# Kernel tuning notes

Hardware: AMD Instinct MI355X
Metric: run time of the kernel (lower is better)

The kernel has to match this reference:

```python
import jax, jax.numpy as jnp
import numpy as np

D_MODEL = 1024
H = 16
D_HEAD = D_MODEL // H  # 64
RANK = 32
ALPHA = 1.0


def _lora_linear(x, W, b, dW, dB):
    # merged weight: W + alpha * (dB @ dW), then x @ W_merged.T + b
    Wm = W + ALPHA * (dB @ dW)
    return x @ Wm.T + b


def setup_inputs() -> dict:
    key = jax.random.key(0)
    ks = jax.random.split(key, 20)
    inp = {"x": jax.random.normal(ks[0], (2, 2048, D_MODEL), dtype=jnp.float32)}
    i = 1
    for name in ("q", "k", "v", "o"):
        inp[f"{name}_W"] = jax.random.normal(ks[i], (D_MODEL, D_MODEL), dtype=jnp.float32) * 0.02; i += 1
        inp[f"{name}_b"] = jnp.zeros((D_MODEL,), dtype=jnp.float32)
        inp[f"{name}_dW"] = jax.random.normal(ks[i], (RANK, D_MODEL), dtype=jnp.float32) * 0.01; i += 1
        inp[f"{name}_dB"] = jax.random.normal(ks[i], (D_MODEL, RANK), dtype=jnp.float32) * 0.01; i += 1
    return inp


def reference(x, q_W, q_b, q_dW, q_dB, k_W, k_b, k_dW, k_dB,
              v_W, v_b, v_dW, v_dB, o_W, o_b, o_dW, o_dB):
    b_s, n, _ = x.shape
    # LoRA-merged QKV projections
    q = _lora_linear(x, q_W, q_b, q_dW, q_dB).reshape(b_s, n, H, D_HEAD)
    k = _lora_linear(x, k_W, k_b, k_dW, k_dB).reshape(b_s, n, H, D_HEAD)
    v = _lora_linear(x, v_W, v_b, v_dW, v_dB).reshape(b_s, n, H, D_HEAD)
    scale = 1.0 / np.sqrt(D_HEAD).astype(np.float32)
    # att: [b, h, nq, nk]
    att = jnp.einsum('bqhd,bkhd->bhqk', q, k) * scale
    att = jax.nn.softmax(att, axis=-1)  # dropout = identity (eval mode)
    out = jnp.einsum('bhqk,bkhd->bqhd', att, v).reshape(b_s, n, H * D_HEAD)
    return _lora_linear(out, o_W, o_b, o_dW, o_dB)
```

## Files before the change

kernel.cpp:

```cpp
#include <hip/hip_runtime.h>

typedef unsigned short ushort_t;
typedef unsigned int u32;
typedef __attribute__((ext_vector_type(8))) short short8;
typedef __attribute__((ext_vector_type(4))) float floatx4;
typedef __attribute__((ext_vector_type(16))) float floatx16;
typedef __attribute__((ext_vector_type(2))) unsigned int uintx2;
typedef __attribute__((ext_vector_type(4))) unsigned int uintx4;

typedef const __attribute__((address_space(1))) u32* gptr_t;
typedef __attribute__((address_space(3))) u32* lptr_t;

__device__ __forceinline__ void async_copy16(void* lds, const void* g) {
  __builtin_amdgcn_global_load_lds((gptr_t)g, (lptr_t)lds, 16, 0, 0);
}

__device__ __forceinline__ ushort_t f2bf(float f) {
  u32 u = __float_as_uint(f);
  u += 0x7fffu + ((u >> 16) & 1u);
  return (ushort_t)(u >> 16);
}

__device__ __forceinline__ floatx4 mfma16(short8 a, short8 b, floatx4 c) {
  return __builtin_amdgcn_mfma_f32_16x16x32_bf16(a, b, c, 0, 0, 0);
}

__device__ __forceinline__ floatx16 mfma32(short8 a, short8 b, floatx16 c) {
  return __builtin_amdgcn_mfma_f32_32x32x16_bf16(a, b, c, 0, 0, 0);
}

__device__ __forceinline__ u32 cvt_pk_bf16(float lo, float hi) {
  u32 r;
  asm("v_cvt_pk_bf16_f32 %0, %1, %2" : "=v"(r) : "v"(lo), "v"(hi));
  return r;
}

__device__ __forceinline__ short8 mkfrag(u32 x0, u32 x1, u32 x2, u32 x3) {
  uintx2 ra = __builtin_amdgcn_permlane32_swap(x0, x2, false, false);
  uintx2 rb = __builtin_amdgcn_permlane32_swap(x1, x3, false, false);
  union { uintx4 u; short8 s; } t;
  t.u[0] = ra[0]; t.u[1] = rb[0]; t.u[2] = ra[1]; t.u[3] = rb[1];
  return t.s;
}

struct alignas(16) F4 { float a, b, c, d; };
struct alignas(8) U4 { ushort_t a, b, c, d; };

#define QSCALE 0.18033688011112043f

__global__ __launch_bounds__(256) void prep_kernel(
    const float* __restrict__ x, ushort_t* __restrict__ xs,
    const float* __restrict__ W0, const float* __restrict__ dW0, const float* __restrict__ dB0,
    const float* __restrict__ W1, const float* __restrict__ dW1, const float* __restrict__ dB1,
    const float* __restrict__ W2, const float* __restrict__ dW2, const float* __restrict__ dB2,
    const float* __restrict__ W3, const float* __restrict__ dW3, const float* __restrict__ dB3,
    ushort_t* __restrict__ Wm) {
  const int bid = blockIdx.x;
  if (bid < 4096) {
    int i = bid * 256 + threadIdx.x;
    F4 v = ((const F4*)x)[i];
    U4 hh = {f2bf(v.a), f2bf(v.b), f2bf(v.c), f2bf(v.d)};
    ((U4*)xs)[i] = hh;
    return;
  }
  const int t = bid - 4096;
  const int layer = t >> 7, sub = t & 127;
  const float* W = (layer == 0) ? W0 : (layer == 1) ? W1 : (layer == 2) ? W2 : W3;
  const float* dW = (layer == 0) ? dW0 : (layer == 1) ? dW1 : (layer == 2) ? dW2 : dW3;
  const float* dB = (layer == 0) ? dB0 : (layer == 1) ? dB1 : (layer == 2) ? dB2 : dB3;
  ushort_t* Wh = Wm + (size_t)layer * 1024 * 1024;
  const int ot = sub * 8;
  const int d0 = threadIdx.x * 4;
  float acc[8][4] = {};
  for (int r = 0; r < 32; ++r) {
    F4 w = *(const F4*)&dW[r * 1024 + d0];
    float wv[4] = {w.a, w.b, w.c, w.d};
#pragma unroll
    for (int o = 0; o < 8; ++o) {
      float s = dB[(ot + o) * 32 + r];
#pragma unroll
      for (int j = 0; j < 4; ++j) acc[o][j] += s * wv[j];
    }
  }
#pragma unroll
  for (int o = 0; o < 8; ++o) {
    F4 w = *(const F4*)&W[(ot + o) * 1024 + d0];
    U4 hh = {f2bf(w.a + acc[o][0]), f2bf(w.b + acc[o][1]),
             f2bf(w.c + acc[o][2]), f2bf(w.d + acc[o][3])};
    *(U4*)&Wh[(ot + o) * 1024 + d0] = hh;
  }
}

template <int MODE, int TN>
__global__ __launch_bounds__(256) void gemm_bt(
    const ushort_t* __restrict__ A, const ushort_t* __restrict__ B,
    const float* __restrict__ b0, const float* __restrict__ b1,
    const float* __restrict__ b2,
    ushort_t* __restrict__ C, ushort_t* __restrict__ vth,
    float* __restrict__ Cf, const int M, const int N, const int K) {
  constexpr int NT2 = TN / 32;
  __shared__ __align__(16) ushort_t lA[2][128 * 32], lB[2][TN * 32];
  const int tid = threadIdx.x;
  const int wave = tid >> 6, lane = tid & 63;
  const int lo4 = lane & 15, quad = lane >> 4;
  const int n0 = blockIdx.x * TN, m0 = blockIdx.y * 128;
  const int wm = (wave >> 1) * 64, wn = (wave & 1) * (TN / 2);

  floatx4 acc[4][NT2];
  const floatx4 zero4 = {0.f, 0.f, 0.f, 0.f};
#pragma unroll
  for (int mt = 0; mt < 4; ++mt)
#pragma unroll
    for (int nt = 0; nt < NT2; ++nt) acc[mt][nt] = zero4;

  const int strow = lane >> 2;
  const int stcol = (lane & 3) * 8;

  const int NTILES = K >> 5;
  {
#pragma unroll
    for (int i = 0; i < 2; ++i) {
      const int g = wave * 2 + i;
      async_copy16(&lA[0][g * 512], A + (size_t)(m0 + g * 16 + strow) * K + stcol);
    }
#pragma unroll
    for (int i = 0; i < TN / 64; ++i) {
      const int g = wave * (TN / 64) + i;
      async_copy16(&lB[0][g * 512], B + (size_t)(n0 + g * 16 + strow) * K + stcol);
    }
  }
  __syncthreads();

  for (int t = 0; t < NTILES; ++t) {
    const int cur = t & 1;
    if (t + 1 < NTILES) {
      const int kk = (t + 1) << 5;
#pragma unroll
      for (int i = 0; i < 2; ++i) {
        const int g = wave * 2 + i;
        async_copy16(&lA[cur ^ 1][g * 512], A + (size_t)(m0 + g * 16 + strow) * K + kk + stcol);
      }
#pragma unroll
      for (int i = 0; i < TN / 64; ++i) {
        const int g = wave * (TN / 64) + i;
        async_copy16(&lB[cur ^ 1][g * 512], B + (size_t)(n0 + g * 16 + strow) * K + kk + stcol);
      }
    }
    short8 a_[4], b_[NT2];
#pragma unroll
    for (int t2 = 0; t2 < 4; ++t2)
      a_[t2] = *(const short8*)&lA[cur][(wm + t2 * 16 + lo4) * 32 + quad * 8];
#pragma unroll
    for (int t2 = 0; t2 < NT2; ++t2)
      b_[t2] = *(const short8*)&lB[cur][(wn + t2 * 16 + lo4) * 32 + quad * 8];
#pragma unroll
    for (int mt = 0; mt < 4; ++mt)
#pragma unroll
      for (int nt = 0; nt < NT2; ++nt) acc[mt][nt] = mfma16(a_[mt], b_[nt], acc[mt][nt]);
    if (t + 1 < NTILES) __syncthreads();
  }

#pragma unroll
  for (int nt = 0; nt < NT2; ++nt) {
    const int col = n0 + wn + nt * 16 + lo4;
    float bias;
    if (MODE == 0)
      bias = (col < 1024) ? b0[col] : (col < 2048) ? b1[col - 1024] : b2[col - 2048];
    else
      bias = b0[col];
#pragma unroll
    for (int mt = 0; mt < 4; ++mt)
#pragma unroll
      for (int r = 0; r < 4; ++r) {
        const int row = m0 + wm + mt * 16 + quad * 4 + r;
        float c = acc[mt][nt][r] + bias;
        if (MODE == 0) {
          if (col < 1024) c *= QSCALE;
          ushort_t hv = f2bf(c);
          if (col < 2048) {
            C[(size_t)row * 2048 + col] = hv;
          } else {
            const int d = col - 2048;
            const size_t vrow = (size_t)(((row >> 11) * 16 + (d >> 6)) * 64 + (d & 63));
            vth[vrow * 2048 + (row & 2047)] = hv;
          }
        } else {
          Cf[(size_t)row * N + col] = c;
        }
      }
  }
}

__global__ __launch_bounds__(256) void attn_kernel(
    const ushort_t* __restrict__ qk, const ushort_t* __restrict__ vt,
    ushort_t* __restrict__ at) {
  __shared__ __align__(16) ushort_t Kh[2][64 * 64];
  __shared__ __align__(16) ushort_t Vh[2][64 * 64];
  const int qt = blockIdx.x, bh = blockIdx.y;
  const int b = bh >> 4, h = bh & 15;
  const int tid = threadIdx.x;
  const int wave = tid >> 6, lane = tid & 63;
  const int l31 = lane & 31, hi = lane >> 5, l7 = lane & 7;

  short8 qf[4];
  {
    const ushort_t* g =
        qk + (size_t)(b * 2048 + qt * 128 + wave * 32 + l31) * 2048 + h * 64 + hi * 8;
#pragma unroll
    for (int st = 0; st < 4; ++st) qf[st] = *(const short8*)(g + st * 16);
  }

  floatx16 O[2];
#pragma unroll
  for (int i = 0; i < 16; ++i) { O[0][i] = 0.f; O[1][i] = 0.f; }
  float l_acc[4] = {0.f, 0.f, 0.f, 0.f};

  const int strow = lane >> 3;
  const int stswz = (l7 ^ strow) * 8;
  const int r0 = wave * 16 + strow, r1 = r0 + 8;
  const int u0 = wave * 1024, u1 = u0 + 512;
  const ushort_t* Ksrc = qk + (size_t)b * 2048 * 2048 + 1024 + h * 64;
  const ushort_t* Vsrc = vt + (size_t)bh * 64 * 2048;

#define STAGE(buf, kt_)                                                  \
  {                                                                      \
    const int kn = (kt_)*64;                                             \
    async_copy16(&Kh[buf][u0], Ksrc + (size_t)(kn + r0) * 2048 + stswz); \
    async_copy16(&Kh[buf][u1], Ksrc + (size_t)(kn + r1) * 2048 + stswz); \
    async_copy16(&Vh[buf][u0], Vsrc + (size_t)r0 * 2048 + kn + stswz);   \
    async_copy16(&Vh[buf][u1], Vsrc + (size_t)r1 * 2048 + kn + stswz);   \
  }

  STAGE(0, 0);
  __syncthreads();

  for (int kt = 0; kt < 32; ++kt) {
    const int cur = kt & 1;
    if (kt + 1 < 32) STAGE(cur ^ 1, kt + 1);

    floatx16 s0, s1;
#pragma unroll
    for (int i = 0; i < 16; ++i) { s0[i] = 0.f; s1[i] = 0.f; }
    __builtin_amdgcn_s_setprio(1);
#pragma unroll
    for (int st = 0; st < 4; ++st) {
      const int c = ((st * 2 + hi) ^ l7) * 8;
      s0 = mfma32(*(const short8*)&Kh[cur][l31 * 64 + c], qf[st], s0);
      s1 = mfma32(*(const short8*)&Kh[cur][(32 + l31) * 64 + c], qf[st], s1);
    }
    __builtin_amdgcn_s_setprio(0);

    u32 a0[8], a1[8];
#pragma unroll
    for (int j = 0; j < 8; ++j) {
      float p0a = __builtin_amdgcn_exp2f(s0[2 * j]);
      float p0b = __builtin_amdgcn_exp2f(s0[2 * j + 1]);
      float p1a = __builtin_amdgcn_exp2f(s1[2 * j]);
      float p1b = __builtin_amdgcn_exp2f(s1[2 * j + 1]);
      l_acc[j & 3] += (p0a + p0b) + (p1a + p1b);
      a0[j] = cvt_pk_bf16(p0a, p0b);
      a1[j] = cvt_pk_bf16(p1a, p1b);
    }

    short8 pb00 = mkfrag(a0[0], a0[1], a0[2], a0[3]);
    short8 pb01 = mkfrag(a0[4], a0[5], a0[6], a0[7]);
    short8 pb10 = mkfrag(a1[0], a1[1], a1[2], a1[3]);
    short8 pb11 = mkfrag(a1[4], a1[5], a1[6], a1[7]);

    __builtin_amdgcn_s_setprio(1);
#pragma unroll
    for (int dblk = 0; dblk < 2; ++dblk) {
      const int vr = (dblk * 32 + l31) * 64;
      O[dblk] = mfma32(*(const short8*)&Vh[cur][vr + ((0 + hi) ^ l7) * 8], pb00, O[dblk]);
      O[dblk] = mfma32(*(const short8*)&Vh[cur][vr + ((2 + hi) ^ l7) * 8], pb01, O[dblk]);
      O[dblk] = mfma32(*(const short8*)&Vh[cur][vr + ((4 + hi) ^ l7) * 8], pb10, O[dblk]);
      O[dblk] = mfma32(*(const short8*)&Vh[cur][vr + ((6 + hi) ^ l7) * 8], pb11, O[dblk]);
    }
    __builtin_amdgcn_s_setprio(0);
    if (kt + 1 < 32) __syncthreads();
  }
#undef STAGE

  float l = (l_acc[0] + l_acc[1]) + (l_acc[2] + l_acc[3]);
  l += __shfl_xor(l, 32);
  const float linv = 1.f / l;
  ushort_t* out = at + (size_t)(b * 2048 + qt * 128 + wave * 32 + l31) * 1024 + h * 64;
#pragma unroll
  for (int dblk = 0; dblk < 2; ++dblk)
#pragma unroll
    for (int g = 0; g < 4; ++g) {
      U4 hh = {f2bf(O[dblk][4 * g + 0] * linv), f2bf(O[dblk][4 * g + 1] * linv),
               f2bf(O[dblk][4 * g + 2] * linv), f2bf(O[dblk][4 * g + 3] * linv)};
      *(U4*)&out[dblk * 32 + g * 8 + hi * 4] = hh;
    }
}

extern "C" void kernel_launch(void* const* d_in, const int* in_sizes, int n_in,
                              void* d_out, int out_size, void* d_ws, size_t ws_size,
                              hipStream_t stream) {
  const float* x = (const float*)d_in[0];
  const float* qW = (const float*)d_in[1];
  const float* qb = (const float*)d_in[2];
  const float* qdW = (const float*)d_in[3];
  const float* qdB = (const float*)d_in[4];
  const float* kW = (const float*)d_in[5];
  const float* kb = (const float*)d_in[6];
  const float* kdW = (const float*)d_in[7];
  const float* kdB = (const float*)d_in[8];
  const float* vW = (const float*)d_in[9];
  const float* vb = (const float*)d_in[10];
  const float* vdW = (const float*)d_in[11];
  const float* vdB = (const float*)d_in[12];
  const float* oW = (const float*)d_in[13];
  const float* ob = (const float*)d_in[14];
  const float* odW = (const float*)d_in[15];
  const float* odB = (const float*)d_in[16];

  char* ws = (char*)d_ws;
  const size_t MB = 1024u * 1024u;
  const size_t WELEM = 1024u * 1024u;
  ushort_t* xs = (ushort_t*)(ws + 0 * MB);
  ushort_t* Wm = (ushort_t*)(ws + 8 * MB);
  ushort_t* qk = (ushort_t*)(ws + 16 * MB);
  ushort_t* vt = (ushort_t*)(ws + 32 * MB);
  ushort_t* at = xs;

  prep_kernel<<<4608, 256, 0, stream>>>(x, xs, qW, qdW, qdB, kW, kdW, kdB,
                                        vW, vdW, vdB, oW, odW, odB, Wm);
  gemm_bt<0, 128><<<dim3(24, 32), 256, 0, stream>>>(xs, Wm, qb, kb, vb,
                                                    qk, vt, nullptr, 4096, 3072, 1024);
  attn_kernel<<<dim3(16, 32), 256, 0, stream>>>(qk, vt, at);
  gemm_bt<1, 64><<<dim3(16, 32), 256, 0, stream>>>(at, Wm + 3 * WELEM, ob, nullptr,
                                                   nullptr, nullptr, nullptr,
                                                   (float*)d_out, 4096, 1024, 1024);
}
```

Before: 227.1 us.

## Load K/V fragments directly from global into registers, drop LDS and barriers

The attention kernel stops staging K and V tiles through LDS with async copies and __syncthreads. Each wave now loads its MFMA operand fragments straight from global memory into registers, double-buffering K across iterations. Other changes: the softmax row sum is computed with MFMA against a ones fragment instead of VALU adds, blocks are remapped so heads group by XCD for L2 locality, and launch bounds request two blocks per CU. This removes LDS traffic and barrier stalls but adds redundant global/L2 reads across the four waves and more register pressure.

Result: slower. 295.7 us (+30.2%).

```diff
diff --git a/kernel.cpp b/kernel.cpp
--- a/kernel.cpp
+++ b/kernel.cpp
@@ -191,107 +191,120 @@
   }
 }
 
-__global__ __launch_bounds__(256) void attn_kernel(
+__global__ __launch_bounds__(256, 2) void attn_kernel(
     const ushort_t* __restrict__ qk, const ushort_t* __restrict__ vt,
     ushort_t* __restrict__ at) {
-  __shared__ __align__(16) ushort_t Kh[2][64 * 64];
-  __shared__ __align__(16) ushort_t Vh[2][64 * 64];
-  const int qt = blockIdx.x, bh = blockIdx.y;
+  const int bid = blockIdx.x;
+  const int xcd = bid & 7, g = bid >> 3;
+  const int bh = xcd * 4 + (g >> 4), qt = g & 15;
   const int b = bh >> 4, h = bh & 15;
   const int tid = threadIdx.x;
   const int wave = tid >> 6, lane = tid & 63;
-  const int l31 = lane & 31, hi = lane >> 5, l7 = lane & 7;
+  const int l31 = lane & 31, hi = lane >> 5;
+  const int hi8 = hi * 8;
+
+  const ushort_t* Kg = qk + (size_t)b * 2048 * 2048 + 1024 + h * 64;
+  const ushort_t* Vg = vt + (size_t)bh * 64 * 2048;
 
   short8 qf[4];
   {
-    const ushort_t* g =
-        qk + (size_t)(b * 2048 + qt * 128 + wave * 32 + l31) * 2048 + h * 64 + hi * 8;
-#pragma unroll
-    for (int st = 0; st < 4; ++st) qf[st] = *(const short8*)(g + st * 16);
-  }
-
-  floatx16 O[2];
-#pragma unroll
-  for (int i = 0; i < 16; ++i) { O[0][i] = 0.f; O[1][i] = 0.f; }
-  float l_acc[4] = {0.f, 0.f, 0.f, 0.f};
-
-  const int strow = lane >> 3;
-  const int stswz = (l7 ^ strow) * 8;
-  const int r0 = wave * 16 + strow, r1 = r0 + 8;
-  const int u0 = wave * 1024, u1 = u0 + 512;
-  const ushort_t* Ksrc = qk + (size_t)b * 2048 * 2048 + 1024 + h * 64;
-  const ushort_t* Vsrc = vt + (size_t)bh * 64 * 2048;
-
-#define STAGE(buf, kt_)                                                  \
-  {                                                                      \
-    const int kn = (kt_)*64;                                             \
-    async_copy16(&Kh[buf][u0], Ksrc + (size_t)(kn + r0) * 2048 + stswz); \
-    async_copy16(&Kh[buf][u1], Ksrc + (size_t)(kn + r1) * 2048 + stswz); \
-    async_copy16(&Vh[buf][u0], Vsrc + (size_t)r0 * 2048 + kn + stswz);   \
-    async_copy16(&Vh[buf][u1], Vsrc + (size_t)r1 * 2048 + kn + stswz);   \
-  }
-
-  STAGE(0, 0);
-  __syncthreads();
-
-  for (int kt = 0; kt < 32; ++kt) {
-    const int cur = kt & 1;
-    if (kt + 1 < 32) STAGE(cur ^ 1, kt + 1);
-
-    floatx16 s0, s1;
-#pragma unroll
-    for (int i = 0; i < 16; ++i) { s0[i] = 0.f; s1[i] = 0.f; }
-    __builtin_amdgcn_s_setprio(1);
-#pragma unroll
-    for (int st = 0; st < 4; ++st) {
-      const int c = ((st * 2 + hi) ^ l7) * 8;
-      s0 = mfma32(*(const short8*)&Kh[cur][l31 * 64 + c], qf[st], s0);
-      s1 = mfma32(*(const short8*)&Kh[cur][(32 + l31) * 64 + c], qf[st], s1);
-    }
-    __builtin_amdgcn_s_setprio(0);
-
-    u32 a0[8], a1[8];
-#pragma unroll
-    for (int j = 0; j < 8; ++j) {
-      float p0a = __builtin_amdgcn_exp2f(s0[2 * j]);
-      float p0b = __builtin_amdgcn_exp2f(s0[2 * j + 1]);
-      float p1a = __builtin_amdgcn_exp2f(s1[2 * j]);
-      float p1b = __builtin_amdgcn_exp2f(s1[2 * j + 1]);
-      l_acc[j & 3] += (p0a + p0b) + (p1a + p1b);
-      a0[j] = cvt_pk_bf16(p0a, p0b);
-      a1[j] = cvt_pk_bf16(p1a, p1b);
-    }
-
-    short8 pb00 = mkfrag(a0[0], a0[1], a0[2], a0[3]);
-    short8 pb01 = mkfrag(a0[4], a0[5], a0[6], a0[7]);
-    short8 pb10 = mkfrag(a1[0], a1[1], a1[2], a1[3]);
-    short8 pb11 = mkfrag(a1[4], a1[5], a1[6], a1[7]);
-
-    __builtin_amdgcn_s_setprio(1);
-#pragma unroll
-    for (int dblk = 0; dblk < 2; ++dblk) {
-      const int vr = (dblk * 32 + l31) * 64;
-      O[dblk] = mfma32(*(const short8*)&Vh[cur][vr + ((0 + hi) ^ l7) * 8], pb00, O[dblk]);
-      O[dblk] = mfma32(*(const short8*)&Vh[cur][vr + ((2 + hi) ^ l7) * 8], pb01, O[dblk]);
-      O[dblk] = mfma32(*(const short8*)&Vh[cur][vr + ((4 + hi) ^ l7) * 8], pb10, O[dblk]);
-      O[dblk] = mfma32(*(const short8*)&Vh[cur][vr + ((6 + hi) ^ l7) * 8], pb11, O[dblk]);
-    }
-    __builtin_amdgcn_s_setprio(0);
-    if (kt + 1 < 32) __syncthreads();
-  }
-#undef STAGE
-
-  float l = (l_acc[0] + l_acc[1]) + (l_acc[2] + l_acc[3]);
-  l += __shfl_xor(l, 32);
-  const float linv = 1.f / l;
+    const ushort_t* gq =
+        qk + (size_t)(b * 2048 + qt * 128 + wave * 32 + l31) * 2048 + h * 64 + hi8;
+#pragma unroll
+    for (int st = 0; st < 4; ++st) qf[st] = *(const short8*)(gq + st * 16);
+  }
+
+  floatx16 O[2], Lacc;
+#pragma unroll
+  for (int i = 0; i < 16; ++i) { O[0][i] = 0.f; O[1][i] = 0.f; Lacc[i] = 0.f; }
+
+  short8 onesf;
+  {
+    union { uintx4 u; short8 s; } ou;
+    ou.u[0] = 0x3F803F80u; ou.u[1] = 0x3F803F80u;
+    ou.u[2] = 0x3F803F80u; ou.u[3] = 0x3F803F80u;
+    onesf = ou.s;
+  }
+
+#define LOADK(dst, kt_)                                                       \
+  {                                                                           \
+    const ushort_t* p_ = Kg + (size_t)(kt_) * 64 * 2048;                      \
+    _Pragma("unroll") for (int st_ = 0; st_ < 4; ++st_) {                     \
+      dst[st_] = *(const short8*)(p_ + (size_t)l31 * 2048 + st_ * 16 + hi8);  \
+      dst[4 + st_] =                                                          \
+          *(const short8*)(p_ + (size_t)(32 + l31) * 2048 + st_ * 16 + hi8); \
+    }                                                                         \
+  }
+
+#define LOADV(dst, kt_)                                                        \
+  {                                                                            \
+    const ushort_t* p_ = Vg + (kt_) * 64 + hi8;                                \
+    _Pragma("unroll") for (int dk_ = 0; dk_ < 2; ++dk_)                        \
+        _Pragma("unroll") for (int ks_ = 0; ks_ < 4; ++ks_)                    \
+            dst[dk_ * 4 + ks_] =                                               \
+                *(const short8*)(p_ + (size_t)(dk_ * 32 + l31) * 2048 + ks_ * 16); \
+  }
+
+#define COMPUTE(kf, vf)                                                     \
+  {                                                                         \
+    floatx16 s0, s1;                                                        \
+    _Pragma("unroll") for (int i_ = 0; i_ < 16; ++i_) {                     \
+      s0[i_] = 0.f; s1[i_] = 0.f;                                           \
+    }                                                                       \
+    __builtin_amdgcn_s_setprio(1);                                          \
+    _Pragma("unroll") for (int st_ = 0; st_ < 4; ++st_) {                   \
+      s0 = mfma32(kf[st_], qf[st_], s0);                                    \
+      s1 = mfma32(kf[4 + st_], qf[st_], s1);                                \
+    }                                                                       \
+    __builtin_amdgcn_s_setprio(0);                                          \
+    u32 a0[8], a1[8];                                                       \
+    _Pragma("unroll") for (int j_ = 0; j_ < 8; ++j_) {                      \
+      a0[j_] = cvt_pk_bf16(__builtin_amdgcn_exp2f(s0[2 * j_]),              \
+                           __builtin_amdgcn_exp2f(s0[2 * j_ + 1]));         \
+      a1[j_] = cvt_pk_bf16(__builtin_amdgcn_exp2f(s1[2 * j_]),              \
+                           __builtin_amdgcn_exp2f(s1[2 * j_ + 1]));         \
+    }                                                                       \
+    short8 pb00 = mkfrag(a0[0], a0[1], a0[2], a0[3]);                       \
+    short8 pb01 = mkfrag(a0[4], a0[5], a0[6], a0[7]);                       \
+    short8 pb10 = mkfrag(a1[0], a1[1], a1[2], a1[3]);                       \
+    short8 pb11 = mkfrag(a1[4], a1[5], a1[6], a1[7]);                       \
+    __builtin_amdgcn_s_setprio(1);                                          \
+    Lacc = mfma32(onesf, pb00, Lacc);                                       \
+    Lacc = mfma32(onesf, pb01, Lacc);                                       \
+    Lacc = mfma32(onesf, pb10, Lacc);                                       \
+    Lacc = mfma32(onesf, pb11, Lacc);                                       \
+    _Pragma("unroll") for (int dk_ = 0; dk_ < 2; ++dk_) {                   \
+      O[dk_] = mfma32(vf[dk_ * 4 + 0], pb00, O[dk_]);                       \
+      O[dk_] = mfma32(vf[dk_ * 4 + 1], pb01, O[dk_]);                       \
+      O[dk_] = mfma32(vf[dk_ * 4 + 2], pb10, O[dk_]);                       \
+      O[dk_] = mfma32(vf[dk_ * 4 + 3], pb11, O[dk_]);                       \
+    }                                                                       \
+    __builtin_amdgcn_s_setprio(0);                                          \
+  }
+
+  short8 kA[8], kB[8], vv[8];
+  LOADK(kA, 0);
+  for (int kt = 0; kt < 32; kt += 2) {
+    LOADV(vv, kt);
+    LOADK(kB, kt + 1);
+    COMPUTE(kA, vv);
+    LOADV(vv, kt + 1);
+    if (kt + 2 < 32) LOADK(kA, kt + 2);
+    COMPUTE(kB, vv);
+  }
+#undef LOADK
+#undef LOADV
+#undef COMPUTE
+
+  const float linv = 1.f / Lacc[0];
   ushort_t* out = at + (size_t)(b * 2048 + qt * 128 + wave * 32 + l31) * 1024 + h * 64;
 #pragma unroll
   for (int dblk = 0; dblk < 2; ++dblk)
 #pragma unroll
-    for (int g = 0; g < 4; ++g) {
-      U4 hh = {f2bf(O[dblk][4 * g + 0] * linv), f2bf(O[dblk][4 * g + 1] * linv),
-               f2bf(O[dblk][4 * g + 2] * linv), f2bf(O[dblk][4 * g + 3] * linv)};
-      *(U4*)&out[dblk * 32 + g * 8 + hi * 4] = hh;
+    for (int gr = 0; gr < 4; ++gr) {
+      U4 hh = {f2bf(O[dblk][4 * gr + 0] * linv), f2bf(O[dblk][4 * gr + 1] * linv),
+               f2bf(O[dblk][4 * gr + 2] * linv), f2bf(O[dblk][4 * gr + 3] * linv)};
+      *(U4*)&out[dblk * 32 + gr * 8 + hi * 4] = hh;
     }
 }
 
@@ -329,7 +342,7 @@
                                         vW, vdW, vdB, oW, odW, odB, Wm);
   gemm_bt<0, 128><<<dim3(24, 32), 256, 0, stream>>>(xs, Wm, qb, kb, vb,
                                                     qk, vt, nullptr, 4096, 3072, 1024);
-  attn_kernel<<<dim3(16, 32), 256, 0, stream>>>(qk, vt, at);
+  attn_kernel<<<512, 256, 0, stream>>>(qk, vt, at);
   gemm_bt<1, 64><<<dim3(16, 32), 256, 0, stream>>>(at, Wm + 3 * WELEM, ob, nullptr,
                                                    nullptr, nullptr, nullptr,
                                                    (float*)d_out, 4096, 1024, 1024);
```

## Split attention key range across two wave halves and remap blocks to XCDs

Applied to the files above, without the earlier changes.

The attention kernel now runs 512 threads per block. The two halves of the waves each process alternating 64-key tiles for the same 128 query rows, so the sequential key loop is half as long per wave. Partial O and row sums are combined through LDS at the end. Blocks are also remapped so that all query tiles of the same batch-head land on the same XCD, which should improve L2 reuse of K/V. The cost is doubled LDS per block, an extra reduction pass and two more barriers. Softmax correctness rests on the existing no-max exp2 scheme, which makes the two partial sums directly additive.

Result: faster. 220.3 us (-3.0%).

```diff
diff --git a/kernel.cpp b/kernel.cpp
--- a/kernel.cpp
+++ b/kernel.cpp
@@ -191,23 +191,27 @@
   }
 }
 
-__global__ __launch_bounds__(256) void attn_kernel(
+__global__ __launch_bounds__(512, 4) void attn_kernel(
     const ushort_t* __restrict__ qk, const ushort_t* __restrict__ vt,
     ushort_t* __restrict__ at) {
-  __shared__ __align__(16) ushort_t Kh[2][64 * 64];
-  __shared__ __align__(16) ushort_t Vh[2][64 * 64];
-  const int qt = blockIdx.x, bh = blockIdx.y;
+  __shared__ __align__(16) ushort_t Kh[2][2][64 * 64];
+  __shared__ __align__(16) ushort_t Vh[2][2][64 * 64];
+  const int bid = blockIdx.x;
+  const int xcd = bid & 7, g = bid >> 3;
+  const int bh = xcd * 4 + (g >> 4), qt = g & 15;
   const int b = bh >> 4, h = bh & 15;
   const int tid = threadIdx.x;
   const int wave = tid >> 6, lane = tid & 63;
+  const int rowg = wave & 3, half = wave >> 2;
   const int l31 = lane & 31, hi = lane >> 5, l7 = lane & 7;
+  const int hi8 = hi * 8;
 
   short8 qf[4];
   {
-    const ushort_t* g =
-        qk + (size_t)(b * 2048 + qt * 128 + wave * 32 + l31) * 2048 + h * 64 + hi * 8;
-#pragma unroll
-    for (int st = 0; st < 4; ++st) qf[st] = *(const short8*)(g + st * 16);
+    const ushort_t* gq =
+        qk + (size_t)(b * 2048 + qt * 128 + rowg * 32 + l31) * 2048 + h * 64 + hi8;
+#pragma unroll
+    for (int st = 0; st < 4; ++st) qf[st] = *(const short8*)(gq + st * 16);
   }
 
   floatx16 O[2];
@@ -215,28 +219,36 @@
   for (int i = 0; i < 16; ++i) { O[0][i] = 0.f; O[1][i] = 0.f; }
   float l_acc[4] = {0.f, 0.f, 0.f, 0.f};
 
+  const int stile = wave >> 1, spart = wave & 1;
   const int strow = lane >> 3;
   const int stswz = (l7 ^ strow) * 8;
-  const int r0 = wave * 16 + strow, r1 = r0 + 8;
-  const int u0 = wave * 1024, u1 = u0 + 512;
   const ushort_t* Ksrc = qk + (size_t)b * 2048 * 2048 + 1024 + h * 64;
   const ushort_t* Vsrc = vt + (size_t)bh * 64 * 2048;
 
-#define STAGE(buf, kt_)                                                  \
-  {                                                                      \
-    const int kn = (kt_)*64;                                             \
-    async_copy16(&Kh[buf][u0], Ksrc + (size_t)(kn + r0) * 2048 + stswz); \
-    async_copy16(&Kh[buf][u1], Ksrc + (size_t)(kn + r1) * 2048 + stswz); \
-    async_copy16(&Vh[buf][u0], Vsrc + (size_t)r0 * 2048 + kn + stswz);   \
-    async_copy16(&Vh[buf][u1], Vsrc + (size_t)r1 * 2048 + kn + stswz);   \
+#define STAGE(buf, t_)                                                             \
+  {                                                                                \
+    const int kt_ = 2 * (t_) + (stile & 1);                                        \
+    if (stile < 2) {                                                               \
+      const ushort_t* s_ =                                                         \
+          Ksrc + (size_t)(kt_ * 64 + spart * 32 + strow) * 2048 + stswz;           \
+      ushort_t* d_ = &Kh[buf][stile & 1][spart * 32 * 64];                         \
+      _Pragma("unroll") for (int i_ = 0; i_ < 4; ++i_)                             \
+          async_copy16(d_ + i_ * 512, s_ + (size_t)i_ * 8 * 2048);                 \
+    } else {                                                                       \
+      const ushort_t* s_ =                                                         \
+          Vsrc + (size_t)(spart * 32 + strow) * 2048 + kt_ * 64 + stswz;           \
+      ushort_t* d_ = &Vh[buf][stile & 1][spart * 32 * 64];                         \
+      _Pragma("unroll") for (int i_ = 0; i_ < 4; ++i_)                             \
+          async_copy16(d_ + i_ * 512, s_ + (size_t)i_ * 8 * 2048);                 \
+    }                                                                              \
   }
 
   STAGE(0, 0);
   __syncthreads();
 
-  for (int kt = 0; kt < 32; ++kt) {
-    const int cur = kt & 1;
-    if (kt + 1 < 32) STAGE(cur ^ 1, kt + 1);
+  for (int t = 0; t < 16; ++t) {
+    const int cur = t & 1;
+    if (t + 1 < 16) STAGE(cur ^ 1, t + 1);
 
     floatx16 s0, s1;
 #pragma unroll
@@ -245,8 +257,8 @@
 #pragma unroll
     for (int st = 0; st < 4; ++st) {
       const int c = ((st * 2 + hi) ^ l7) * 8;
-      s0 = mfma32(*(const short8*)&Kh[cur][l31 * 64 + c], qf[st], s0);
-      s1 = mfma32(*(const short8*)&Kh[cur][(32 + l31) * 64 + c], qf[st], s1);
+      s0 = mfma32(*(const short8*)&Kh[cur][half][l31 * 64 + c], qf[st], s0);
+      s1 = mfma32(*(const short8*)&Kh[cur][half][(32 + l31) * 64 + c], qf[st], s1);
     }
     __builtin_amdgcn_s_setprio(0);
 
@@ -271,28 +283,50 @@
 #pragma unroll
     for (int dblk = 0; dblk < 2; ++dblk) {
       const int vr = (dblk * 32 + l31) * 64;
-      O[dblk] = mfma32(*(const short8*)&Vh[cur][vr + ((0 + hi) ^ l7) * 8], pb00, O[dblk]);
-      O[dblk] = mfma32(*(const short8*)&Vh[cur][vr + ((2 + hi) ^ l7) * 8], pb01, O[dblk]);
-      O[dblk] = mfma32(*(const short8*)&Vh[cur][vr + ((4 + hi) ^ l7) * 8], pb10, O[dblk]);
-      O[dblk] = mfma32(*(const short8*)&Vh[cur][vr + ((6 + hi) ^ l7) * 8], pb11, O[dblk]);
+      O[dblk] = mfma32(*(const short8*)&Vh[cur][half][vr + ((0 + hi) ^ l7) * 8], pb00, O[dblk]);
+      O[dblk] = mfma32(*(const short8*)&Vh[cur][half][vr + ((2 + hi) ^ l7) * 8], pb01, O[dblk]);
+      O[dblk] = mfma32(*(const short8*)&Vh[cur][half][vr + ((4 + hi) ^ l7) * 8], pb10, O[dblk]);
+      O[dblk] = mfma32(*(const short8*)&Vh[cur][half][vr + ((6 + hi) ^ l7) * 8], pb11, O[dblk]);
     }
     __builtin_amdgcn_s_setprio(0);
-    if (kt + 1 < 32) __syncthreads();
+    if (t + 1 < 16) __syncthreads();
   }
 #undef STAGE
 
   float l = (l_acc[0] + l_acc[1]) + (l_acc[2] + l_acc[3]);
   l += __shfl_xor(l, 32);
-  const float linv = 1.f / l;
-  ushort_t* out = at + (size_t)(b * 2048 + qt * 128 + wave * 32 + l31) * 1024 + h * 64;
-#pragma unroll
-  for (int dblk = 0; dblk < 2; ++dblk)
-#pragma unroll
-    for (int g = 0; g < 4; ++g) {
-      U4 hh = {f2bf(O[dblk][4 * g + 0] * linv), f2bf(O[dblk][4 * g + 1] * linv),
-               f2bf(O[dblk][4 * g + 2] * linv), f2bf(O[dblk][4 * g + 3] * linv)};
-      *(U4*)&out[dblk * 32 + g * 8 + hi * 4] = hh;
-    }
+
+  float* Pf0 = (float*)&Kh[0][0][0];
+  float* Pf1 = (float*)&Vh[0][0][0];
+  __syncthreads();
+  if (half == 1) {
+    const int base = rowg * 1280 + lane * 20;
+#pragma unroll
+    for (int j = 0; j < 16; ++j) Pf0[base + j] = O[0][j];
+#pragma unroll
+    for (int j = 0; j < 16; ++j) Pf1[base + j] = O[1][j];
+    Pf0[base + 16] = l;
+  }
+  __syncthreads();
+  if (half == 0) {
+    const int base = rowg * 1280 + lane * 20;
+#pragma unroll
+    for (int j = 0; j < 16; ++j) O[0][j] += Pf0[base + j];
+#pragma unroll
+    for (int j = 0; j < 16; ++j) O[1][j] += Pf1[base + j];
+    l += Pf0[base + 16];
+    const float linv = 1.f / l;
+    ushort_t* out =
+        at + (size_t)(b * 2048 + qt * 128 + rowg * 32 + l31) * 1024 + h * 64;
+#pragma unroll
+    for (int dblk = 0; dblk < 2; ++dblk)
+#pragma unroll
+      for (int gr = 0; gr < 4; ++gr) {
+        U4 hh = {f2bf(O[dblk][4 * gr + 0] * linv), f2bf(O[dblk][4 * gr + 1] * linv),
+                 f2bf(O[dblk][4 * gr + 2] * linv), f2bf(O[dblk][4 * gr + 3] * linv)};
+        *(U4*)&out[dblk * 32 + gr * 8 + hi * 4] = hh;
+      }
+  }
 }
 
 extern "C" void kernel_launch(void* const* d_in, const int* in_sizes, int n_in,
@@ -329,7 +363,7 @@
                                         vW, vdW, vdB, oW, odW, odB, Wm);
   gemm_bt<0, 128><<<dim3(24, 32), 256, 0, stream>>>(xs, Wm, qb, kb, vb,
                                                     qk, vt, nullptr, 4096, 3072, 1024);
-  attn_kernel<<<dim3(16, 32), 256, 0, stream>>>(qk, vt, at);
+  attn_kernel<<<512, 512, 0, stream>>>(qk, vt, at);
   gemm_bt<1, 64><<<dim3(16, 32), 256, 0, stream>>>(at, Wm + 3 * WELEM, ob, nullptr,
                                                    nullptr, nullptr, nullptr,
                                                    (float*)d_out, 4096, 1024, 1024);
```
